# Performance work log

Measured on AMD Instinct MI355X. Metric: run time of the kernel, lower is better.

Reference implementation:

```python
import jax, jax.numpy as jnp
import numpy as np

NH, NP = 4, 4  # num_heads, num_points (num_levels = 1)
LN_EPS = 1e-5


def _layernorm(t, g, b):
    m = t.mean(-1, keepdims=True)
    v = t.var(-1, keepdims=True)
    return (t - m) / jnp.sqrt(v + LN_EPS) * g + b


def setup_inputs() -> dict:
    key = jax.random.key(0)
    ks = jax.random.split(key, 12)
    C, B, H, W = 256, 2, 128, 128
    s = 0.02
    w = lambda k, shape: jax.random.normal(k, shape, jnp.float32) * s
    return {
        "x": jax.random.normal(ks[0], (B, C, H, W), jnp.float32),
        "norm_g": jnp.ones((C,), jnp.float32),
        "norm_b": jnp.zeros((C,), jnp.float32),
        "ffn_g": jnp.ones((C,), jnp.float32),
        "ffn_b": jnp.zeros((C,), jnp.float32),
        "W_val": w(ks[1], (C, C)),
        "b_val": jnp.zeros((C,), jnp.float32),
        "W_off": w(ks[2], (NH * NP * 2, C)),
        "b_off": jax.random.normal(ks[3], (NH * NP * 2,), jnp.float32),
        "W_attn": w(ks[4], (NH * NP, C)),
        "b_attn": jnp.zeros((NH * NP,), jnp.float32),
        "W_out": w(ks[5], (C, C)),
        "b_out": jnp.zeros((C,), jnp.float32),
        "dw_w": w(ks[6], (C, 1, 3, 3)),
        "dw_b": jnp.zeros((C,), jnp.float32),
        "pr_w": w(ks[7], (C, C // 2)),
        "pr_b": jnp.zeros((C,), jnp.float32),
    }


def reference(x, norm_g, norm_b, ffn_g, ffn_b, W_val, b_val, W_off, b_off,
              W_attn, b_attn, W_out, b_out, dw_w, dw_b, pr_w, pr_b):
    B, C, H, W = x.shape
    D = C // NH
    N = H * W
    xf = x.reshape(B, C, N).transpose(0, 2, 1)  # [B, N, C]
    q = _layernorm(xf, norm_g, norm_b)           # query == value (pre-norm)

    value = (q @ W_val.T + b_val).reshape(B, N, NH, D)
    off = (q @ W_off.T + b_off).reshape(B, N, NH, NP, 2)
    aw = jax.nn.softmax((q @ W_attn.T + b_attn).reshape(B, N, NH, NP), axis=-1)

    # reference points: normalized pixel centers (x, y) in [0, 1]
    gx = (jnp.arange(W, dtype=x.dtype) + 0.5) / W
    gy = (jnp.arange(H, dtype=x.dtype) + 0.5) / H
    my, mx = jnp.meshgrid(gy, gx, indexing='ij')
    ref = jnp.stack([mx.reshape(-1), my.reshape(-1)], axis=-1)  # [N, 2]

    offset_norm = jnp.array([W, H], x.dtype)
    loc = ref[None, :, None, None, :] + off / offset_norm  # [B,N,NH,NP,2]

    # grid_sample bilinear, align_corners=False, zero padding
    px = loc[..., 0] * W - 0.5
    py = loc[..., 1] * H - 0.5
    x0 = jnp.floor(px)
    y0 = jnp.floor(py)
    wx = (px - x0).transpose(0, 2, 1, 3)[..., None]  # [B,NH,N,NP,1]
    wy = (py - y0).transpose(0, 2, 1, 3)[..., None]
    x0i = x0.astype(jnp.int32)
    y0i = y0.astype(jnp.int32)

    vt = value.transpose(0, 2, 1, 3)  # [B, NH, N, D]

    def gather(xi, yi):
        valid = ((xi >= 0) & (xi < W) & (yi >= 0) & (yi < H)).astype(x.dtype)
        idx = jnp.clip(yi, 0, H - 1) * W + jnp.clip(xi, 0, W - 1)  # [B,N,NH,NP]
        it = idx.transpose(0, 2, 1, 3).reshape(B, NH, N * NP, 1)
        g = jnp.take_along_axis(vt, it, axis=2).reshape(B, NH, N, NP, D)
        return g * valid.transpose(0, 2, 1, 3)[..., None]

    v00 = gather(x0i, y0i)
    v01 = gather(x0i + 1, y0i)
    v10 = gather(x0i, y0i + 1)
    v11 = gather(x0i + 1, y0i + 1)
    sampled = (v00 * (1 - wx) * (1 - wy) + v01 * wx * (1 - wy)
               + v10 * (1 - wx) * wy + v11 * wx * wy)  # [B,NH,N,NP,D]

    attn_out = (sampled * aw.transpose(0, 2, 1, 3)[..., None]).sum(3)  # [B,NH,N,D]
    attn_out = attn_out.transpose(0, 2, 1, 3).reshape(B, N, C)
    out = attn_out @ W_out.T + b_out + xf  # residual (identity), dropout=0

    res = out
    y = _layernorm(out, ffn_g, ffn_b)
    yi = y.transpose(0, 2, 1).reshape(B, C, H, W)
    dw = jax.lax.conv_general_dilated(
        yi, dw_w, (1, 1), 'SAME', feature_group_count=C,
        dimension_numbers=('NCHW', 'OIHW', 'NCHW')) + dw_b[None, :, None, None]
    x1, x2 = dw[:, :C // 2], dw[:, C // 2:]
    h = jax.nn.silu(x1) * x2  # [B, C/2, H, W]
    pr = jnp.einsum('bchw,oc->bohw', h, pr_w) + pr_b[None, :, None, None]
    return pr + res.transpose(0, 2, 1).reshape(B, C, H, W)
```

## Files before the change

### kernel.cpp

```cpp
#include <hip/hip_runtime.h>
#include <cmath>

typedef unsigned short u16;
typedef __attribute__((ext_vector_type(8))) short short8v;
typedef __attribute__((ext_vector_type(4))) float f32x4;

#define C_DIM 256
#define H_DIM 128
#define W_DIM 128
#define N_DIM (H_DIM*W_DIM)
#define B_DIM 2
#define LN_EPSF 1e-5f

__device__ __forceinline__ u16 f2b(float f) {
  unsigned u = __float_as_uint(f);
  unsigned r = (u + 0x7fffu + ((u >> 16) & 1u)) >> 16;
  return (u16)r;
}
__device__ __forceinline__ float b2f(u16 h) {
  return __uint_as_float(((unsigned)h) << 16);
}

__global__ __launch_bounds__(256) void k_cvt5(const float* __restrict__ w0,
      const float* __restrict__ w1, const float* __restrict__ w2,
      const float* __restrict__ w3, const float* __restrict__ w4,
      u16* __restrict__ d0, u16* __restrict__ d1, u16* __restrict__ d2,
      u16* __restrict__ d3) {
  int i = blockIdx.x*256 + threadIdx.x;
  const float* s; u16* d; int l;
  if (i < 16384)      { s = w0; d = d0;        l = i; }
  else if (i < 32768) { s = w1; d = d1;        l = i - 16384; }
  else if (i < 40960) { s = w2; d = d2;        l = i - 32768; }
  else if (i < 43008) { s = w3; d = d3;        l = i - 40960; }
  else if (i < 44032) { s = w4; d = d3 + 8192; l = i - 43008; }
  else return;
  float4 v = *(const float4*)&s[(size_t)l*4];
  d[l*4+0]=f2b(v.x); d[l*4+1]=f2b(v.y); d[l*4+2]=f2b(v.z); d[l*4+3]=f2b(v.w);
}

__global__ __launch_bounds__(256) void k_fused1(const float* __restrict__ x,
      const float* __restrict__ g, const float* __restrict__ bta,
      const u16* __restrict__ wv, const float* __restrict__ bval,
      const u16* __restrict__ wab, const float* __restrict__ boff,
      const float* __restrict__ battn,
      u16* __restrict__ val, float* __restrict__ off, float* __restrict__ aw) {
  __shared__ float tile[256*33];
  __shared__ float psum[256], psq[256];
  __shared__ float rmean[32], rstd[32];
  __shared__ u16 qls[64*256];
  int t = threadIdx.x;
  int blk = blockIdx.x;
  int b = blk >> 8;
  int n0 = (blk & 255) * 64;
  for (int half = 0; half < 2; ++half) {
    int nh0 = n0 + half*32;
    int nl = t & 31, cr = t >> 5;
    #pragma unroll 4
    for (int i = 0; i < 32; ++i) {
      int c = i*8 + cr;
      tile[c*33 + nl] = x[((size_t)(b*C_DIM + c))*N_DIM + nh0 + nl];
    }
    __syncthreads();
    {
      int n = t & 31, j = t >> 5;
      float s = 0.f, s2 = 0.f;
      #pragma unroll 8
      for (int i = 0; i < 32; ++i) {
        float v = tile[(j*32+i)*33 + n];
        s += v; s2 += v*v;
      }
      psum[j*32+n] = s; psq[j*32+n] = s2;
    }
    __syncthreads();
    if (t < 32) {
      float s=0.f, s2=0.f;
      for (int j=0;j<8;++j){ s += psum[j*32+t]; s2 += psq[j*32+t]; }
      float m = s * (1.f/256.f);
      float var = s2 * (1.f/256.f) - m*m;
      rmean[t] = m; rstd[t] = rsqrtf(var + LN_EPSF);
    }
    __syncthreads();
    float gt = g[t], bt = bta[t];
    #pragma unroll 4
    for (int i = 0; i < 32; ++i) {
      float v = tile[t*33 + i];
      int n = half*32 + i;
      qls[n*256 + (t ^ ((n & 7) << 3))] = f2b((v - rmean[i]) * rstd[i] * gt + bt);
    }
    __syncthreads();
  }
  int lane = t & 63, w = t >> 6;
  int l15 = lane & 15, lk = (lane >> 4) * 8;
  f32x4 acc[4][4] = {};
  f32x4 acc_oa[4] = {};
  float bias_v[4];
  #pragma unroll
  for (int oj = 0; oj < 4; ++oj) bias_v[oj] = bval[w*64 + oj*16 + l15];
  #pragma unroll
  for (int k0 = 0; k0 < 256; k0 += 32) {
    short8v af[4], bf[4];
    #pragma unroll
    for (int mi = 0; mi < 4; ++mi) {
      int n = mi*16 + l15;
      af[mi] = *(const short8v*)&qls[n*256 + ((k0 + lk) ^ ((n & 7) << 3))];
    }
    #pragma unroll
    for (int oj = 0; oj < 4; ++oj)
      bf[oj] = *(const short8v*)&wv[(size_t)(w*64 + oj*16 + l15)*256 + k0 + lk];
    #pragma unroll
    for (int mi = 0; mi < 4; ++mi)
      #pragma unroll
      for (int oj = 0; oj < 4; ++oj)
        acc[mi][oj] = __builtin_amdgcn_mfma_f32_16x16x32_bf16(af[mi], bf[oj], acc[mi][oj], 0,0,0);
    if (w < 3) {
      short8v bw = *(const short8v*)&wab[(size_t)(w*16 + l15)*256 + k0 + lk];
      #pragma unroll
      for (int mi = 0; mi < 4; ++mi)
        acc_oa[mi] = __builtin_amdgcn_mfma_f32_16x16x32_bf16(af[mi], bw, acc_oa[mi], 0,0,0);
    }
  }
  int rbase = (lane >> 4) * 4;
  #pragma unroll
  for (int mi = 0; mi < 4; ++mi)
    #pragma unroll
    for (int oj = 0; oj < 4; ++oj)
      #pragma unroll
      for (int r = 0; r < 4; ++r) {
        size_t m = (size_t)(b*N_DIM + n0 + mi*16 + rbase + r);
        int o = w*64 + oj*16 + l15;
        val[m*256 + o] = f2b(acc[mi][oj][r] + bias_v[oj]);
      }
  if (w < 2) {
    int o = w*16 + l15;
    float bv2 = boff[o];
    #pragma unroll
    for (int mi = 0; mi < 4; ++mi)
      #pragma unroll
      for (int r = 0; r < 4; ++r) {
        size_t m = (size_t)(b*N_DIM + n0 + mi*16 + rbase + r);
        off[m*32 + o] = acc_oa[mi][r] + bv2;
      }
  } else if (w == 2) {
    float bv2 = battn[l15];
    #pragma unroll
    for (int mi = 0; mi < 4; ++mi)
      #pragma unroll
      for (int r = 0; r < 4; ++r) {
        float v = acc_oa[mi][r] + bv2;
        float mx = fmaxf(v, __shfl_xor(v, 1));
        mx = fmaxf(mx, __shfl_xor(mx, 2));
        float e = expf(v - mx);
        float s = e + __shfl_xor(e, 1);
        s = s + __shfl_xor(s, 2);
        size_t m = (size_t)(b*N_DIM + n0 + mi*16 + rbase + r);
        aw[m*16 + l15] = e / s;
      }
  }
}

__global__ __launch_bounds__(256) void k_sample_ln(const u16* __restrict__ value,
      const float* __restrict__ off, const float* __restrict__ aw,
      const u16* __restrict__ wo, const float* __restrict__ bo,
      const float* __restrict__ x,
      const float* __restrict__ g, const float* __restrict__ bta,
      u16* __restrict__ yt, u16* __restrict__ res) {
  __shared__ u16 sls[64*256];
  __shared__ float rmean[64], rstd[64];
  int t = threadIdx.x;
  int lane = t & 63, w = t >> 6;
  int blk = blockIdx.x;
  int b = blk >> 8;
  int n0 = (blk & 255) * 64;
  int nh = lane >> 4;
  int dg = (lane & 15) * 4;
  #pragma unroll 1
  for (int it = 0; it < 16; ++it) {
    int rl = it*4 + w;
    int ng = n0 + rl;
    size_t bn = (size_t)b*N_DIM + ng;
    int hc = ng >> 7, wc = ng & 127;
    int vbase = b*(N_DIM*256) + nh*64 + dg;
    const float* op = &off[bn*32 + nh*8];
    const float* ap = &aw[bn*16 + nh*4];
    float acc0=0.f, acc1=0.f, acc2=0.f, acc3=0.f;
    #pragma unroll
    for (int p = 0; p < 4; ++p) {
      float ox = op[p*2+0], oy = op[p*2+1];
      float a  = ap[p];
      float px = (float)wc + ox;
      float py = (float)hc + oy;
      float x0f = floorf(px), y0f = floorf(py);
      float wx = px - x0f, wy = py - y0f;
      int x0 = (int)x0f, y0 = (int)y0f;
      int x1 = x0 + 1, y1 = y0 + 1;
      float fx0 = (1.f - wx) * ((x0 >= 0 && x0 < W_DIM) ? 1.f : 0.f);
      float fx1 = wx         * ((x1 >= 0 && x1 < W_DIM) ? 1.f : 0.f);
      float fy0 = a * (1.f - wy) * ((y0 >= 0 && y0 < H_DIM) ? 1.f : 0.f);
      float fy1 = a * wy         * ((y1 >= 0 && y1 < H_DIM) ? 1.f : 0.f);
      int xc0 = min(max(x0,0),W_DIM-1), xc1 = min(max(x1,0),W_DIM-1);
      int yc0 = min(max(y0,0),H_DIM-1), yc1 = min(max(y1,0),H_DIM-1);
      int r0 = yc0*W_DIM, r1 = yc1*W_DIM;
      {
        ushort4 v = *(const ushort4*)&value[vbase + (r0+xc0)*256];
        float wgt = fx0*fy0;
        acc0 += wgt*b2f(v.x); acc1 += wgt*b2f(v.y); acc2 += wgt*b2f(v.z); acc3 += wgt*b2f(v.w);
      }
      {
        ushort4 v = *(const ushort4*)&value[vbase + (r0+xc1)*256];
        float wgt = fx1*fy0;
        acc0 += wgt*b2f(v.x); acc1 += wgt*b2f(v.y); acc2 += wgt*b2f(v.z); acc3 += wgt*b2f(v.w);
      }
      {
        ushort4 v = *(const ushort4*)&value[vbase + (r1+xc0)*256];
        float wgt = fx0*fy1;
        acc0 += wgt*b2f(v.x); acc1 += wgt*b2f(v.y); acc2 += wgt*b2f(v.z); acc3 += wgt*b2f(v.w);
      }
      {
        ushort4 v = *(const ushort4*)&value[vbase + (r1+xc1)*256];
        float wgt = fx1*fy1;
        acc0 += wgt*b2f(v.x); acc1 += wgt*b2f(v.y); acc2 += wgt*b2f(v.z); acc3 += wgt*b2f(v.w);
      }
    }
    ushort4 o4;
    o4.x = f2b(acc0); o4.y = f2b(acc1); o4.z = f2b(acc2); o4.w = f2b(acc3);
    int k = nh*64 + dg;
    *(ushort4*)&sls[rl*256 + (k ^ ((rl & 7) << 3))] = o4;
  }
  __syncthreads();
  int l15 = lane & 15, lk = (lane >> 4) * 8;
  int rbase = (lane >> 4) * 4;
  f32x4 acc[4][4] = {};
  float bias_v[4], gv[4], btv[4];
  #pragma unroll
  for (int oj = 0; oj < 4; ++oj) {
    int o = w*64 + oj*16 + l15;
    bias_v[oj] = bo[o]; gv[oj] = g[o]; btv[oj] = bta[o];
  }
  #pragma unroll
  for (int k0 = 0; k0 < 256; k0 += 32) {
    short8v af[4], bf[4];
    #pragma unroll
    for (int mi = 0; mi < 4; ++mi) {
      int n = mi*16 + l15;
      af[mi] = *(const short8v*)&sls[n*256 + ((k0 + lk) ^ ((n & 7) << 3))];
    }
    #pragma unroll
    for (int oj = 0; oj < 4; ++oj)
      bf[oj] = *(const short8v*)&wo[(size_t)(w*64 + oj*16 + l15)*256 + k0 + lk];
    #pragma unroll
    for (int mi = 0; mi < 4; ++mi)
      #pragma unroll
      for (int oj = 0; oj < 4; ++oj)
        acc[mi][oj] = __builtin_amdgcn_mfma_f32_16x16x32_bf16(af[mi], bf[oj], acc[mi][oj], 0,0,0);
  }
  #pragma unroll
  for (int mi = 0; mi < 4; ++mi)
    #pragma unroll
    for (int oj = 0; oj < 4; ++oj) {
      int o = w*64 + oj*16 + l15;
      const float* xp = &x[((size_t)(b*256 + o))*N_DIM + n0 + mi*16 + rbase];
      #pragma unroll
      for (int r = 0; r < 4; ++r)
        acc[mi][oj][r] += bias_v[oj] + xp[r];
    }
  __syncthreads();
  float* pred = (float*)sls;
  int cidx = w*16 + l15;
  #pragma unroll
  for (int mi = 0; mi < 4; ++mi)
    #pragma unroll
    for (int r = 0; r < 4; ++r) {
      int row = mi*16 + rbase + r;
      float s  = acc[mi][0][r] + acc[mi][1][r] + acc[mi][2][r] + acc[mi][3][r];
      float s2 = acc[mi][0][r]*acc[mi][0][r] + acc[mi][1][r]*acc[mi][1][r]
               + acc[mi][2][r]*acc[mi][2][r] + acc[mi][3][r]*acc[mi][3][r];
      pred[row*64 + cidx] = s;
      pred[4096 + row*64 + cidx] = s2;
    }
  __syncthreads();
  {
    int row = t >> 2, q = t & 3;
    float s = 0.f, s2 = 0.f;
    #pragma unroll
    for (int i = 0; i < 16; ++i) {
      s  += pred[row*64 + q*16 + i];
      s2 += pred[4096 + row*64 + q*16 + i];
    }
    s  += __shfl_xor(s, 1);  s  += __shfl_xor(s, 2);
    s2 += __shfl_xor(s2, 1); s2 += __shfl_xor(s2, 2);
    if (q == 0) {
      float m = s * (1.f/256.f);
      float var = s2 * (1.f/256.f) - m*m;
      rmean[row] = m; rstd[row] = rsqrtf(var + LN_EPSF);
    }
  }
  __syncthreads();
  #pragma unroll
  for (int mi = 0; mi < 4; ++mi)
    #pragma unroll
    for (int oj = 0; oj < 4; ++oj) {
      int o = w*64 + oj*16 + l15;
      size_t base = ((size_t)(b*256 + o))*N_DIM + n0 + mi*16 + rbase;
      ushort4 rv, yv;
      u16 rr[4], yy[4];
      #pragma unroll
      for (int r = 0; r < 4; ++r) {
        int row = mi*16 + rbase + r;
        float v = acc[mi][oj][r];
        rr[r] = f2b(v);
        yy[r] = f2b((v - rmean[row]) * rstd[row] * gv[oj] + btv[oj]);
      }
      rv.x=rr[0]; rv.y=rr[1]; rv.z=rr[2]; rv.w=rr[3];
      yv.x=yy[0]; yv.y=yy[1]; yv.z=yy[2]; yv.w=yy[3];
      *(ushort4*)&res[base] = rv;
      *(ushort4*)&yt[base]  = yv;
    }
}

__global__ __launch_bounds__(256) void k_dwconv(const u16* __restrict__ yt,
     const float* __restrict__ dww, const float* __restrict__ dwb,
     u16* __restrict__ hb) {
  int t = threadIdx.x;
  int blk = blockIdx.x;
  int ht = blk & 63; int c = (blk >> 6) & 127; int b = blk >> 13;
  int hh = t >> 7; int ww = t & 127;
  int h = ht*2 + hh;
  const u16* p1 = yt + ((size_t)(b*256 + c))*N_DIM;
  const u16* p2 = yt + ((size_t)(b*256 + c + 128))*N_DIM;
  float w1[9], w2[9];
  #pragma unroll
  for (int i=0;i<9;++i){ w1[i]=dww[c*9+i]; w2[i]=dww[(c+128)*9+i]; }
  float a1 = dwb[c], a2 = dwb[c+128];
  #pragma unroll
  for (int ky=0;ky<3;++ky){
    int yy = h + ky - 1;
    if (yy < 0 || yy >= H_DIM) continue;
    #pragma unroll
    for (int kx=0;kx<3;++kx){
      int xx = ww + kx - 1;
      if (xx < 0 || xx >= W_DIM) continue;
      float v1 = b2f(p1[yy*W_DIM+xx]), v2 = b2f(p2[yy*W_DIM+xx]);
      a1 += w1[ky*3+kx]*v1; a2 += w2[ky*3+kx]*v2;
    }
  }
  float sig = 1.f/(1.f+expf(-a1));
  hb[((size_t)(b*128+c))*N_DIM + h*W_DIM + ww] = f2b(a1*sig*a2);
}

__global__ __launch_bounds__(256) void k_prfinal_mfma(const u16* __restrict__ hsrc,
     const u16* __restrict__ pw, const float* __restrict__ prb,
     const u16* __restrict__ resb, float* __restrict__ dout) {
  __shared__ u16 hls[64*128];
  int t = threadIdx.x;
  int lane = t & 63, w = t >> 6;
  int b = blockIdx.y;
  int n0 = blockIdx.x * 64;
  #pragma unroll
  for (int r = 0; r < 4; ++r) {
    int e = t + 256*r;
    int k = e >> 3;
    int n8 = (e & 7) * 8;
    short8v v = *(const short8v*)&hsrc[((size_t)(b*128 + k))*N_DIM + n0 + n8];
    #pragma unroll
    for (int j = 0; j < 8; ++j) {
      int n = n8 + j;
      hls[n*128 + (k ^ ((n & 7) << 3))] = (u16)v[j];
    }
  }
  __syncthreads();
  int l15 = lane & 15, lk = (lane >> 4) * 8;
  f32x4 acc[4][4] = {};
  #pragma unroll
  for (int k0 = 0; k0 < 128; k0 += 32) {
    short8v af[4], bf[4];
    #pragma unroll
    for (int oi = 0; oi < 4; ++oi)
      af[oi] = *(const short8v*)&pw[(size_t)(w*64 + oi*16 + l15)*128 + k0 + lk];
    #pragma unroll
    for (int nj = 0; nj < 4; ++nj) {
      int n = nj*16 + l15;
      bf[nj] = *(const short8v*)&hls[n*128 + ((k0 + lk) ^ ((n & 7) << 3))];
    }
    #pragma unroll
    for (int oi = 0; oi < 4; ++oi)
      #pragma unroll
      for (int nj = 0; nj < 4; ++nj)
        acc[oi][nj] = __builtin_amdgcn_mfma_f32_16x16x32_bf16(af[oi], bf[nj], acc[oi][nj], 0,0,0);
  }
  int rbase = (lane >> 4) * 4;
  #pragma unroll
  for (int oi = 0; oi < 4; ++oi)
    #pragma unroll
    for (int r = 0; r < 4; ++r) {
      int o = w*64 + oi*16 + rbase + r;
      float pb = prb[o];
      #pragma unroll
      for (int nj = 0; nj < 4; ++nj) {
        int n = n0 + nj*16 + l15;
        size_t idx = ((size_t)(b*256 + o))*N_DIM + n;
        dout[idx] = acc[oi][nj][r] + pb + b2f(resb[idx]);
      }
    }
}

extern "C" void kernel_launch(void* const* d_in, const int* in_sizes, int n_in,
                              void* d_out, int out_size, void* d_ws, size_t ws_size,
                              hipStream_t stream) {
  const float* x      = (const float*)d_in[0];
  const float* norm_g = (const float*)d_in[1];
  const float* norm_b = (const float*)d_in[2];
  const float* ffn_g  = (const float*)d_in[3];
  const float* ffn_b  = (const float*)d_in[4];
  const float* W_val  = (const float*)d_in[5];
  const float* b_val  = (const float*)d_in[6];
  const float* W_off  = (const float*)d_in[7];
  const float* b_off  = (const float*)d_in[8];
  const float* W_attn = (const float*)d_in[9];
  const float* b_attn = (const float*)d_in[10];
  const float* W_out  = (const float*)d_in[11];
  const float* b_out  = (const float*)d_in[12];
  const float* dw_w   = (const float*)d_in[13];
  const float* dw_b   = (const float*)d_in[14];
  const float* pr_w   = (const float*)d_in[15];
  const float* pr_b   = (const float*)d_in[16];
  float* outp = (float*)d_out;

  char* ws = (char*)d_ws;
  const size_t MB = 1u << 20;
  u16*   valbf  = (u16*)(ws);
  u16*   resbf  = (u16*)(ws + 17*MB);
  u16*   ytbf   = (u16*)(ws + 34*MB);
  u16*   hbuf   = (u16*)(ws + 51*MB);
  float* boffb  = (float*)(ws + 64*MB);
  float* bawb   = (float*)(ws + 69*MB);
  u16*   wvbf   = (u16*)(ws + 72*MB);
  u16*   wobf   = (u16*)(ws + 72*MB + 131072u);
  u16*   pwbf   = (u16*)(ws + 72*MB + 262144u);
  u16*   wabbf  = (u16*)(ws + 72*MB + 327680u);

  k_cvt5<<<dim3(172), dim3(256), 0, stream>>>(W_val, W_out, pr_w, W_off, W_attn,
                                              wvbf, wobf, pwbf, wabbf);
  k_fused1<<<dim3(512), dim3(256), 0, stream>>>(x, norm_g, norm_b, wvbf, b_val,
                                                wabbf, b_off, b_attn,
                                                valbf, boffb, bawb);
  k_sample_ln<<<dim3(512), dim3(256), 0, stream>>>(valbf, boffb, bawb, wobf, b_out,
                                                   x, ffn_g, ffn_b, ytbf, resbf);
  k_dwconv<<<dim3(16384), dim3(256), 0, stream>>>(ytbf, dw_w, dw_b, hbuf);
  k_prfinal_mfma<<<dim3(256, 2), dim3(256), 0, stream>>>(hbuf, pwbf, pr_b, resbf, outp);

  (void)in_sizes; (void)n_in; (void)out_size; (void)ws_size;
}
```

Measured before the change: 134.6 us.

## Split deformable sampling from out-projection LayerNorm into separate kernels

The fused sample+out-proj+LN kernel is split in two. A standalone sampling kernel runs one wave per pixel over 8192 blocks, with a remapped block order, and writes bf16 attention output to a new workspace buffer. A second kernel reads it for the MFMA projection and LayerNorm. The goal is far more parallelism for the latency-bound gather, which ran as a serial 16-iteration loop inside only 512 blocks. The cost is an extra global write and read of a 16 MB intermediate plus one more kernel launch.

```diff
diff --git a/kernel.cpp b/kernel.cpp
--- a/kernel.cpp
+++ b/kernel.cpp
@@ -158,75 +158,77 @@
   }
 }
 
-__global__ __launch_bounds__(256) void k_sample_ln(const u16* __restrict__ value,
+__global__ __launch_bounds__(256) void k_sample(const u16* __restrict__ value,
       const float* __restrict__ off, const float* __restrict__ aw,
+      u16* __restrict__ attn_out) {
+  int t = threadIdx.x;
+  int wv = t >> 6, lane = t & 63;
+  int orig = blockIdx.x;
+  int id = (orig & 7) * 1024 + (orig >> 3);
+  int bn = id*4 + wv;
+  int b = bn >> 14, n = bn & (N_DIM-1);
+  int hc = n >> 7, wc = n & 127;
+  int nh = lane >> 4;
+  int dg = (lane & 15) * 4;
+  int vbase = b*(N_DIM*256) + nh*64 + dg;
+  const float* op = &off[(size_t)bn*32 + nh*8];
+  const float* ap = &aw[(size_t)bn*16 + nh*4];
+  float acc0=0.f, acc1=0.f, acc2=0.f, acc3=0.f;
+  #pragma unroll
+  for (int p = 0; p < 4; ++p) {
+    float ox = op[p*2+0], oy = op[p*2+1];
+    float a  = ap[p];
+    float px = (float)wc + ox;
+    float py = (float)hc + oy;
+    float x0f = floorf(px), y0f = floorf(py);
+    float wx = px - x0f, wy = py - y0f;
+    int x0 = (int)x0f, y0 = (int)y0f;
+    int x1 = x0 + 1, y1 = y0 + 1;
+    float fx0 = (1.f - wx) * ((x0 >= 0 && x0 < W_DIM) ? 1.f : 0.f);
+    float fx1 = wx         * ((x1 >= 0 && x1 < W_DIM) ? 1.f : 0.f);
+    float fy0 = a * (1.f - wy) * ((y0 >= 0 && y0 < H_DIM) ? 1.f : 0.f);
+    float fy1 = a * wy         * ((y1 >= 0 && y1 < H_DIM) ? 1.f : 0.f);
+    int xc0 = min(max(x0,0),W_DIM-1), xc1 = min(max(x1,0),W_DIM-1);
+    int yc0 = min(max(y0,0),H_DIM-1), yc1 = min(max(y1,0),H_DIM-1);
+    int r0 = yc0*W_DIM, r1 = yc1*W_DIM;
+    {
+      ushort4 v = *(const ushort4*)&value[vbase + (r0+xc0)*256];
+      float wgt = fx0*fy0;
+      acc0 += wgt*b2f(v.x); acc1 += wgt*b2f(v.y); acc2 += wgt*b2f(v.z); acc3 += wgt*b2f(v.w);
+    }
+    {
+      ushort4 v = *(const ushort4*)&value[vbase + (r0+xc1)*256];
+      float wgt = fx1*fy0;
+      acc0 += wgt*b2f(v.x); acc1 += wgt*b2f(v.y); acc2 += wgt*b2f(v.z); acc3 += wgt*b2f(v.w);
+    }
+    {
+      ushort4 v = *(const ushort4*)&value[vbase + (r1+xc0)*256];
+      float wgt = fx0*fy1;
+      acc0 += wgt*b2f(v.x); acc1 += wgt*b2f(v.y); acc2 += wgt*b2f(v.z); acc3 += wgt*b2f(v.w);
+    }
+    {
+      ushort4 v = *(const ushort4*)&value[vbase + (r1+xc1)*256];
+      float wgt = fx1*fy1;
+      acc0 += wgt*b2f(v.x); acc1 += wgt*b2f(v.y); acc2 += wgt*b2f(v.z); acc3 += wgt*b2f(v.w);
+    }
+  }
+  ushort4 o;
+  o.x = f2b(acc0); o.y = f2b(acc1); o.z = f2b(acc2); o.w = f2b(acc3);
+  *(ushort4*)&attn_out[(size_t)bn*256 + nh*64 + dg] = o;
+}
+
+__global__ __launch_bounds__(256) void k_out_ln(const u16* __restrict__ ain,
       const u16* __restrict__ wo, const float* __restrict__ bo,
       const float* __restrict__ x,
       const float* __restrict__ g, const float* __restrict__ bta,
       u16* __restrict__ yt, u16* __restrict__ res) {
-  __shared__ u16 sls[64*256];
+  __shared__ float pred[8192];
   __shared__ float rmean[64], rstd[64];
   int t = threadIdx.x;
   int lane = t & 63, w = t >> 6;
   int blk = blockIdx.x;
   int b = blk >> 8;
   int n0 = (blk & 255) * 64;
-  int nh = lane >> 4;
-  int dg = (lane & 15) * 4;
-  #pragma unroll 1
-  for (int it = 0; it < 16; ++it) {
-    int rl = it*4 + w;
-    int ng = n0 + rl;
-    size_t bn = (size_t)b*N_DIM + ng;
-    int hc = ng >> 7, wc = ng & 127;
-    int vbase = b*(N_DIM*256) + nh*64 + dg;
-    const float* op = &off[bn*32 + nh*8];
-    const float* ap = &aw[bn*16 + nh*4];
-    float acc0=0.f, acc1=0.f, acc2=0.f, acc3=0.f;
-    #pragma unroll
-    for (int p = 0; p < 4; ++p) {
-      float ox = op[p*2+0], oy = op[p*2+1];
-      float a  = ap[p];
-      float px = (float)wc + ox;
-      float py = (float)hc + oy;
-      float x0f = floorf(px), y0f = floorf(py);
-      float wx = px - x0f, wy = py - y0f;
-      int x0 = (int)x0f, y0 = (int)y0f;
-      int x1 = x0 + 1, y1 = y0 + 1;
-      float fx0 = (1.f - wx) * ((x0 >= 0 && x0 < W_DIM) ? 1.f : 0.f);
-      float fx1 = wx         * ((x1 >= 0 && x1 < W_DIM) ? 1.f : 0.f);
-      float fy0 = a * (1.f - wy) * ((y0 >= 0 && y0 < H_DIM) ? 1.f : 0.f);
-      float fy1 = a * wy         * ((y1 >= 0 && y1 < H_DIM) ? 1.f : 0.f);
-      int xc0 = min(max(x0,0),W_DIM-1), xc1 = min(max(x1,0),W_DIM-1);
-      int yc0 = min(max(y0,0),H_DIM-1), yc1 = min(max(y1,0),H_DIM-1);
-      int r0 = yc0*W_DIM, r1 = yc1*W_DIM;
-      {
-        ushort4 v = *(const ushort4*)&value[vbase + (r0+xc0)*256];
-        float wgt = fx0*fy0;
-        acc0 += wgt*b2f(v.x); acc1 += wgt*b2f(v.y); acc2 += wgt*b2f(v.z); acc3 += wgt*b2f(v.w);
-      }
-      {
-        ushort4 v = *(const ushort4*)&value[vbase + (r0+xc1)*256];
-        float wgt = fx1*fy0;
-        acc0 += wgt*b2f(v.x); acc1 += wgt*b2f(v.y); acc2 += wgt*b2f(v.z); acc3 += wgt*b2f(v.w);
-      }
-      {
-        ushort4 v = *(const ushort4*)&value[vbase + (r1+xc0)*256];
-        float wgt = fx0*fy1;
-        acc0 += wgt*b2f(v.x); acc1 += wgt*b2f(v.y); acc2 += wgt*b2f(v.z); acc3 += wgt*b2f(v.w);
-      }
-      {
-        ushort4 v = *(const ushort4*)&value[vbase + (r1+xc1)*256];
-        float wgt = fx1*fy1;
-        acc0 += wgt*b2f(v.x); acc1 += wgt*b2f(v.y); acc2 += wgt*b2f(v.z); acc3 += wgt*b2f(v.w);
-      }
-    }
-    ushort4 o4;
-    o4.x = f2b(acc0); o4.y = f2b(acc1); o4.z = f2b(acc2); o4.w = f2b(acc3);
-    int k = nh*64 + dg;
-    *(ushort4*)&sls[rl*256 + (k ^ ((rl & 7) << 3))] = o4;
-  }
-  __syncthreads();
   int l15 = lane & 15, lk = (lane >> 4) * 8;
   int rbase = (lane >> 4) * 4;
   f32x4 acc[4][4] = {};
@@ -240,10 +242,8 @@
   for (int k0 = 0; k0 < 256; k0 += 32) {
     short8v af[4], bf[4];
     #pragma unroll
-    for (int mi = 0; mi < 4; ++mi) {
-      int n = mi*16 + l15;
-      af[mi] = *(const short8v*)&sls[n*256 + ((k0 + lk) ^ ((n & 7) << 3))];
-    }
+    for (int mi = 0; mi < 4; ++mi)
+      af[mi] = *(const short8v*)&ain[(size_t)(b*N_DIM + n0 + mi*16 + l15)*256 + k0 + lk];
     #pragma unroll
     for (int oj = 0; oj < 4; ++oj)
       bf[oj] = *(const short8v*)&wo[(size_t)(w*64 + oj*16 + l15)*256 + k0 + lk];
@@ -263,8 +263,6 @@
       for (int r = 0; r < 4; ++r)
         acc[mi][oj][r] += bias_v[oj] + xp[r];
     }
-  __syncthreads();
-  float* pred = (float*)sls;
   int cidx = w*16 + l15;
   #pragma unroll
   for (int mi = 0; mi < 4; ++mi)
@@ -428,23 +426,25 @@
   char* ws = (char*)d_ws;
   const size_t MB = 1u << 20;
   u16*   valbf  = (u16*)(ws);
-  u16*   resbf  = (u16*)(ws + 17*MB);
-  u16*   ytbf   = (u16*)(ws + 34*MB);
-  u16*   hbuf   = (u16*)(ws + 51*MB);
-  float* boffb  = (float*)(ws + 64*MB);
-  float* bawb   = (float*)(ws + 69*MB);
-  u16*   wvbf   = (u16*)(ws + 72*MB);
-  u16*   wobf   = (u16*)(ws + 72*MB + 131072u);
-  u16*   pwbf   = (u16*)(ws + 72*MB + 262144u);
-  u16*   wabbf  = (u16*)(ws + 72*MB + 327680u);
+  u16*   attnbf = (u16*)(ws + 17*MB);
+  u16*   resbf  = (u16*)(ws + 34*MB);
+  u16*   ytbf   = (u16*)(ws + 51*MB);
+  u16*   hbuf   = (u16*)(ws + 68*MB);
+  float* boffb  = (float*)(ws + 77*MB);
+  float* bawb   = (float*)(ws + 82*MB);
+  u16*   wvbf   = (u16*)(ws + 85*MB);
+  u16*   wobf   = (u16*)(ws + 85*MB + 131072u);
+  u16*   pwbf   = (u16*)(ws + 85*MB + 262144u);
+  u16*   wabbf  = (u16*)(ws + 85*MB + 327680u);
 
   k_cvt5<<<dim3(172), dim3(256), 0, stream>>>(W_val, W_out, pr_w, W_off, W_attn,
                                               wvbf, wobf, pwbf, wabbf);
   k_fused1<<<dim3(512), dim3(256), 0, stream>>>(x, norm_g, norm_b, wvbf, b_val,
                                                 wabbf, b_off, b_attn,
                                                 valbf, boffb, bawb);
-  k_sample_ln<<<dim3(512), dim3(256), 0, stream>>>(valbf, boffb, bawb, wobf, b_out,
-                                                   x, ffn_g, ffn_b, ytbf, resbf);
+  k_sample<<<dim3(8192), dim3(256), 0, stream>>>(valbf, boffb, bawb, attnbf);
+  k_out_ln<<<dim3(512), dim3(256), 0, stream>>>(attnbf, wobf, b_out,
+                                                x, ffn_g, ffn_b, ytbf, resbf);
   k_dwconv<<<dim3(16384), dim3(256), 0, stream>>>(ytbf, dw_w, dw_b, hbuf);
   k_prfinal_mfma<<<dim3(256, 2), dim3(256), 0, stream>>>(hbuf, pwbf, pr_b, resbf, outp);
 
```

Result: faster. 128.4 us (-4.6%).
